# Performance work log

Measured on AMD Instinct MI355X. Metric: run time of the kernel, lower is better.

Reference implementation:

```python
import jax, jax.numpy as jnp
import numpy as np

B, T, S, D, H = 2, 2048, 2048, 2048, 16
HD = D // H  # 128
SCALE = 1.0 / np.sqrt(HD)


def _rope(x, cos, sin):
    # x: [B,H,S,HD]; cos/sin: [1,1,S,HD//2]
    b, h, s, d = x.shape
    xs = x.reshape(b, h, s, d // 2, 2)
    x0, x1 = xs[..., 0], xs[..., 1]
    rot = jnp.stack([x0 * cos - x1 * sin, x1 * cos + x0 * sin], axis=-1)
    return rot.reshape(b, h, s, d)


def _split_heads(x):
    b, s, _ = x.shape
    return x.reshape(b, s, H, HD).transpose(0, 2, 1, 3)


def setup_inputs() -> dict:
    key = jax.random.key(0)
    ks = jax.random.split(key, 6)
    w_std = (1.0 / np.sqrt(2.0)) * np.sqrt(6.0 / (D + D))  # xavier_uniform with gain 1/sqrt(2)
    def xavier(k):
        return jax.random.uniform(k, (D, D), jnp.float32, -w_std, w_std)
    # rotary tables (standard inv-freq form)
    inv_freq = 1.0 / (10000.0 ** (np.arange(0, HD, 2, dtype=np.float32) / HD))  # [HD//2]
    ang = np.arange(T, dtype=np.float32)[:, None] * inv_freq[None, :]           # [T,HD//2]
    cos = jnp.asarray(np.cos(ang), jnp.float32)[None, None]  # [1,1,T,HD//2]
    sin = jnp.asarray(np.sin(ang), jnp.float32)[None, None]
    return {
        "hidden_states": jax.random.normal(ks[0], (B, T, D), jnp.float32),
        "encoder_hidden_states": jax.random.normal(ks[1], (B, S, D), jnp.float32),
        "Wq": xavier(ks[2]),
        "Wk": xavier(ks[3]),
        "Wv": xavier(ks[4]),
        "Wo": xavier(ks[5]),
        "cos_q": cos, "sin_q": sin,
        "cos_k": cos, "sin_k": sin,
    }


def reference(hidden_states, encoder_hidden_states, Wq, Wk, Wv, Wo,
              cos_q, sin_q, cos_k, sin_k):
    # Linear (no bias): y = x @ W.T
    q = _split_heads(jnp.einsum('btd,ed->bte', hidden_states, Wq))          # [B,H,T,HD]
    k = _split_heads(jnp.einsum('bsd,ed->bse', encoder_hidden_states, Wk))  # [B,H,S,HD]
    v = _split_heads(jnp.einsum('bsd,ed->bse', encoder_hidden_states, Wv))  # [B,H,S,HD]
    q = _rope(q, cos_q, sin_q)
    k = _rope(k, cos_k, sin_k)
    scores = jnp.einsum('bhtd,bhsd->bhts', q, k) * SCALE                    # [B,H,T,S]
    attn = jax.nn.softmax(scores.astype(jnp.float32), axis=-1)
    ctx = jnp.einsum('bhts,bhsd->bhtd', attn, v)                            # [B,H,T,HD]
    ctx = ctx.transpose(0, 2, 1, 3).reshape(B, T, D)                        # merge heads
    return jnp.einsum('btd,ed->bte', ctx, Wo)
```

## Files before the change

### kernel.cpp

```cpp
#include <hip/hip_runtime.h>
#include <cmath>

#define SCALE_F 0.088388347648318447f

typedef _Float16 f16;
typedef _Float16 f16x8 __attribute__((ext_vector_type(8)));
typedef _Float16 f16x4 __attribute__((ext_vector_type(4)));
typedef float f32x4 __attribute__((ext_vector_type(4)));
typedef float f32x16 __attribute__((ext_vector_type(16)));
typedef unsigned int u32;
typedef unsigned int u32x4 __attribute__((ext_vector_type(4)));

#define MFMA16(a, b, c) __builtin_amdgcn_mfma_f32_16x16x32_f16(a, b, c, 0, 0, 0)
#define MFMA32(a, b, c) __builtin_amdgcn_mfma_f32_32x32x16_f16(a, b, c, 0, 0, 0)
#define Z16 ((f32x16){0.f,0.f,0.f,0.f,0.f,0.f,0.f,0.f,0.f,0.f,0.f,0.f,0.f,0.f,0.f,0.f})

__device__ __forceinline__ void gl2lds16(const f16* g, f16* l) {
    __builtin_amdgcn_global_load_lds(
        (const __attribute__((address_space(1))) unsigned int*)g,
        (__attribute__((address_space(3))) unsigned int*)l, 16, 0, 0);
}

__device__ __forceinline__ u32 pk2(float x, float y) {
    const unsigned short a = __builtin_bit_cast(unsigned short, (f16)x);
    const unsigned short b = __builtin_bit_cast(unsigned short, (f16)y);
    return (u32)a | ((u32)b << 16);
}
__device__ __forceinline__ float fswapsum(float x) {
    u32 a = __builtin_bit_cast(u32, x), b;
    asm volatile("v_mov_b32 %0, %1" : "=&v"(b) : "v"(a));
    asm volatile("v_permlane32_swap_b32 %0, %1" : "+v"(a), "+v"(b));
    return __builtin_bit_cast(float, a) + __builtin_bit_cast(float, b);
}
__device__ __forceinline__ float fswapmax(float x) {
    u32 a = __builtin_bit_cast(u32, x), b;
    asm volatile("v_mov_b32 %0, %1" : "=&v"(b) : "v"(a));
    asm volatile("v_permlane32_swap_b32 %0, %1" : "+v"(a), "+v"(b));
    return fmaxf(__builtin_bit_cast(float, a), __builtin_bit_cast(float, b));
}

__global__ __launch_bounds__(256) void cvt_all(
    const float* __restrict__ hs, const float* __restrict__ es,
    const float* __restrict__ Wq, const float* __restrict__ Wk,
    const float* __restrict__ Wv, const float* __restrict__ Wo,
    f16* __restrict__ dst)
{
    const int c = blockIdx.x * 256 + threadIdx.x;
    const float* src; int off;
    if (c < 2097152) { src = (c < 1048576) ? hs : es; off = c & 1048575; }
    else {
        const int cc = c - 2097152;
        const int wsel = cc >> 19; off = cc & 524287;
        src = wsel == 0 ? Wq : wsel == 1 ? Wk : wsel == 2 ? Wv : Wo;
    }
    const float4* p = (const float4*)src + (size_t)off * 2;
    const float4 a = p[0], b2 = p[1];
    f16x8 o = {(f16)a.x, (f16)a.y, (f16)a.z, (f16)a.w,
               (f16)b2.x, (f16)b2.y, (f16)b2.z, (f16)b2.w};
    *(f16x8*)(dst + (size_t)c * 8) = o;
}

template <int OUT_MODE>
__global__ __launch_bounds__(256, 2) void gemm16(
    const f16* __restrict__ A, const f16* __restrict__ W,
    void* __restrict__ Cv, int M, int N, int K,
    const float* __restrict__ Cs, const float* __restrict__ Sn)
{
    __shared__ __align__(16) f16 Al[128 * 64];
    __shared__ __align__(16) f16 Bl[128 * 64];
    const int tid = threadIdx.x;
    const int l = tid & 63, w = tid >> 6;
    const int wr = w >> 1, wc = w & 1;

    const int nwg = gridDim.x, cpx = nwg >> 3;
    const int bid = blockIdx.x;
    const int swz = (bid & 7) * cpx + (bid >> 3);
    const int nbn = N >> 7;
    const int bm = (swz / nbn) * 128, bn = (swz % nbn) * 128;

    f32x4 acc[4][4];
#pragma unroll
    for (int i = 0; i < 4; ++i)
#pragma unroll
        for (int j = 0; j < 4; ++j) acc[i][j] = (f32x4){0.f, 0.f, 0.f, 0.f};

    const int srow = tid >> 3;
    const int sg = tid & 7;

    for (int k0 = 0; k0 < K; k0 += 64) {
        __syncthreads();
#pragma unroll
        for (int i = 0; i < 4; ++i) {
            const int row = i * 32 + srow;
            const int lg = sg ^ (row & 7);
            gl2lds16(A + (size_t)(bm + row) * K + k0 + lg * 8, Al + row * 64 + sg * 8);
            gl2lds16(W + (size_t)(bn + row) * K + k0 + lg * 8, Bl + row * 64 + sg * 8);
        }
        __syncthreads();
#pragma unroll
        for (int kk = 0; kk < 2; ++kk) {
            f16x8 a[4], b[4];
            const int g = kk * 4 + (l >> 4);
#pragma unroll
            for (int m = 0; m < 4; ++m) {
                const int row = wr * 64 + m * 16 + (l & 15);
                a[m] = *(const f16x8*)(Al + row * 64 + (g ^ (row & 7)) * 8);
            }
#pragma unroll
            for (int n = 0; n < 4; ++n) {
                const int row = wc * 64 + n * 16 + (l & 15);
                b[n] = *(const f16x8*)(Bl + row * 64 + (g ^ (row & 7)) * 8);
            }
#pragma unroll
            for (int m = 0; m < 4; ++m)
#pragma unroll
                for (int n = 0; n < 4; ++n)
                    acc[m][n] = MFMA16(a[m], b[n], acc[m][n]);
        }
    }

#pragma unroll
    for (int m = 0; m < 4; ++m)
#pragma unroll
        for (int n = 0; n < 4; ++n)
#pragma unroll
            for (int j = 0; j < 4; ++j) {
                const int r = bm + wr * 64 + m * 16 + ((l >> 4) << 2) + j;
                const int c = bn + wc * 64 + n * 16 + (l & 15);
                if (OUT_MODE == 0) {
                    ((f16*)Cv)[(size_t)r * N + c] = (f16)acc[m][n][j];
                } else if (OUT_MODE == 2) {
                    ((float*)Cv)[(size_t)r * N + c] = acc[m][n][j];
                } else if (OUT_MODE == 3) {
                    ((f16*)Cv)[(size_t)((c >> 11) * 2048 + r) * 2048 + (c & 2047)] = (f16)acc[m][n][j];
                } else if (OUT_MODE == 4) {
                    const float v = acc[m][n][j];
                    const float vp = __shfl_xor(v, 1);
                    const int t = r & 2047;
                    const int i2 = (c & 127) >> 1;
                    const float co = Cs[t * 64 + i2];
                    const float si = Sn[t * 64 + i2];
                    const float y = (c & 1) ? fmaf(v, co, vp * si) : fmaf(v, co, -vp * si);
                    ((f16*)Cv)[(size_t)r * N + c] = (f16)y;
                }
            }
}

__global__ __launch_bounds__(512, 1) void attn16(
    const f16* __restrict__ Qg, const f16* __restrict__ Kg,
    const f16* __restrict__ Vt, f16* __restrict__ Og)
{
    __shared__ __align__(16) f16 Kl[2][64 * 128];
    __shared__ __align__(16) f16 Vl[2][128 * 64];
    __shared__ float bnc[8][32];

    const int tid = threadIdx.x;
    const int l = tid & 63, w = tid >> 6;
    const int l31 = l & 31, hi = l >> 5;
    const int hi4 = hi * 4;

    const int bid = blockIdx.x;
    const int swz = (bid & 7) * 32 + (bid >> 3);
    const int bh = swz >> 3, qt = swz & 7;
    const int b = bh >> 4, h = bh & 15;

    const int qrow = b * 2048 + qt * 256 + w * 32 + l31;
    const f16 qsc = (f16)(0.088388347648318447f * 1.44269504088896f);
    f16x8 qf[8];
#pragma unroll
    for (int kc = 0; kc < 8; ++kc) {
        f16x8 t0 = *(const f16x8*)(Qg + (size_t)qrow * 2048 + h * 128 + kc * 16 + hi * 8);
#pragma unroll
        for (int e = 0; e < 8; ++e) t0[e] = t0[e] * qsc;
        qf[kc] = t0;
    }

    f32x16 o[4] = {Z16, Z16, Z16, Z16};
    float mrow = -3.0e38f, lrow = 0.0f;

    const f16* Kbase = Kg + (size_t)(b * 2048) * 2048 + h * 128;
    const f16* Vbase = Vt + (size_t)(b * 2048 + h * 128) * 2048;

#define STAGE(buf, st) do {                                                              \
    _Pragma("unroll")                                                                    \
    for (int u = 0; u < 2; ++u) {                                                        \
        const int idx = u * 512 + tid; const int row = idx >> 4, g = idx & 15;           \
        gl2lds16(Kbase + (size_t)((st) + row) * 2048 + (g ^ (row & 15)) * 8,             \
                 &Kl[buf][row * 128 + g * 8]);                                           \
    }                                                                                    \
    _Pragma("unroll")                                                                    \
    for (int u = 0; u < 2; ++u) {                                                        \
        const int idx = u * 512 + tid; const int d = idx >> 3, g = idx & 7;              \
        gl2lds16(Vbase + (size_t)d * 2048 + (st) + (g ^ (d & 7)) * 8,                    \
                 &Vl[buf][d * 64 + g * 8]);                                              \
    }                                                                                    \
} while (0)

    STAGE(0, 0);
    __syncthreads();

    int cur = 0;
    for (int t = 0; t < 32; ++t) {
        if (t < 31) STAGE(cur ^ 1, (t + 1) * 64);
        const f16* Kc = Kl[cur];
        const f16* Vc = Vl[cur];

        f32x16 p0 = Z16, p1 = Z16;
        __builtin_amdgcn_s_setprio(1);
#pragma unroll
        for (int kc = 0; kc < 8; ++kc) {
            const int g = ((kc * 2 + hi) ^ (l31 & 15)) * 8;
            const f16x8 k0 = *(const f16x8*)(Kc + l31 * 128 + g);
            const f16x8 k1 = *(const f16x8*)(Kc + (32 + l31) * 128 + g);
            p0 = MFMA32(k0, qf[kc], p0);
            p1 = MFMA32(k1, qf[kc], p1);
        }
        __builtin_amdgcn_s_setprio(0);

        float mx = fmaxf(p0[0], p1[0]);
#pragma unroll
        for (int r = 1; r < 16; ++r) mx = fmaxf(mx, fmaxf(p0[r], p1[r]));
        mx = fswapmax(mx);

        if (!__all(mx <= mrow + 8.0f)) {
            const float mn = fmaxf(mrow, mx);
            const float cr = exp2f(mrow - mn);
            mrow = mn;
            lrow *= cr;
            if (hi == 0) bnc[w][l31] = cr;
#pragma unroll
            for (int r = 0; r < 16; ++r) {
                const float crr = bnc[w][(r & 3) + 8 * (r >> 2) + 4 * hi];
                o[0][r] *= crr; o[1][r] *= crr; o[2][r] *= crr; o[3][r] *= crr;
            }
        }

        float s0 = 0.f, s1 = 0.f, s2 = 0.f, s3 = 0.f;
#pragma unroll
        for (int r = 0; r < 16; r += 4) {
            p0[r]     = exp2f(p0[r]     - mrow); s0 += p0[r];
            p0[r + 1] = exp2f(p0[r + 1] - mrow); s1 += p0[r + 1];
            p0[r + 2] = exp2f(p0[r + 2] - mrow); s2 += p0[r + 2];
            p0[r + 3] = exp2f(p0[r + 3] - mrow); s3 += p0[r + 3];
        }
#pragma unroll
        for (int r = 0; r < 16; r += 4) {
            p1[r]     = exp2f(p1[r]     - mrow); s0 += p1[r];
            p1[r + 1] = exp2f(p1[r + 1] - mrow); s1 += p1[r + 1];
            p1[r + 2] = exp2f(p1[r + 2] - mrow); s2 += p1[r + 2];
            p1[r + 3] = exp2f(p1[r + 3] - mrow); s3 += p1[r + 3];
        }
        lrow += fswapsum((s0 + s1) + (s2 + s3));

        f16x8 pf[4];
#pragma unroll
        for (int ksl = 0; ksl < 2; ++ksl) {
            u32x4 w0 = {pk2(p0[8*ksl+0], p0[8*ksl+1]), pk2(p0[8*ksl+2], p0[8*ksl+3]),
                        pk2(p0[8*ksl+4], p0[8*ksl+5]), pk2(p0[8*ksl+6], p0[8*ksl+7])};
            pf[ksl] = __builtin_bit_cast(f16x8, w0);
            u32x4 w1 = {pk2(p1[8*ksl+0], p1[8*ksl+1]), pk2(p1[8*ksl+2], p1[8*ksl+3]),
                        pk2(p1[8*ksl+4], p1[8*ksl+5]), pk2(p1[8*ksl+6], p1[8*ksl+7])};
            pf[2 + ksl] = __builtin_bit_cast(f16x8, w1);
        }

        __builtin_amdgcn_s_setprio(1);
#pragma unroll
        for (int dt = 0; dt < 4; ++dt) {
            const f16* vrow = Vc + (dt * 32 + l31) * 64;
#pragma unroll
            for (int ks = 0; ks < 4; ++ks) {
                const f16x4 vlo = *(const f16x4*)(vrow + ((ks * 2)     ^ (l31 & 7)) * 8 + hi4);
                const f16x4 vhi = *(const f16x4*)(vrow + ((ks * 2 + 1) ^ (l31 & 7)) * 8 + hi4);
                const f16x8 vf = __builtin_shufflevector(vlo, vhi, 0, 1, 2, 3, 4, 5, 6, 7);
                o[dt] = MFMA32(pf[ks], vf, o[dt]);
            }
        }
        __builtin_amdgcn_s_setprio(0);

        __syncthreads();
        cur ^= 1;
    }
#undef STAGE

    const float inv = 1.0f / lrow;
    if (hi == 0) bnc[w][l31] = inv;
#pragma unroll
    for (int r = 0; r < 16; ++r) {
        const int qq = (r & 3) + 8 * (r >> 2) + 4 * hi;
        const float ir = bnc[w][qq];
        const size_t row = (size_t)(b * 2048 + qt * 256 + w * 32 + qq);
#pragma unroll
        for (int dt = 0; dt < 4; ++dt)
            Og[row * 2048 + h * 128 + dt * 32 + l31] = (f16)(o[dt][r] * ir);
    }
}

extern "C" void kernel_launch(void* const* d_in, const int* in_sizes, int n_in,
                              void* d_out, int out_size, void* d_ws, size_t ws_size,
                              hipStream_t stream) {
    const float* hs = (const float*)d_in[0];
    const float* es = (const float*)d_in[1];
    const float* Wq = (const float*)d_in[2];
    const float* Wk = (const float*)d_in[3];
    const float* Wv = (const float*)d_in[4];
    const float* Wo = (const float*)d_in[5];
    const float* cq = (const float*)d_in[6];
    const float* sq = (const float*)d_in[7];
    const float* ck = (const float*)d_in[8];
    const float* sk = (const float*)d_in[9];
    float* out = (float*)d_out;

    f16* hs16 = (f16*)d_ws;
    f16* es16 = hs16 + 8388608;
    f16* Wq16 = es16 + 8388608;
    f16* Wk16 = Wq16 + 4194304;
    f16* Wv16 = Wk16 + 4194304;
    f16* Wo16 = Wv16 + 4194304;
    f16* Q16  = Wo16 + 4194304;
    f16* K16  = Q16 + 8388608;
    f16* Vt16 = K16 + 8388608;
    f16* ctx16 = hs16;

    const dim3 tB(256);
    cvt_all<<<dim3(16384), tB, 0, stream>>>(hs, es, Wq, Wk, Wv, Wo, hs16);

    gemm16<4><<<dim3(512), tB, 0, stream>>>(hs16, Wq16, Q16, 4096, 2048, 2048, cq, sq);
    gemm16<4><<<dim3(512), tB, 0, stream>>>(es16, Wk16, K16, 4096, 2048, 2048, ck, sk);
    gemm16<3><<<dim3(512), tB, 0, stream>>>(Wv16, es16, Vt16, 2048, 4096, 2048, nullptr, nullptr);

    attn16<<<dim3(256), dim3(512), 0, stream>>>(Q16, K16, Vt16, ctx16);

    gemm16<2><<<dim3(512), tB, 0, stream>>>(ctx16, Wo16, out, 4096, 2048, 2048, nullptr, nullptr);
}
```

Measured before the change: 303.9 us.

## Shrink attention blocks to 4 waves, two per CU, and use native exp2

The attention kernel now launches 512 blocks of 256 threads, each covering 128 query rows instead of 256, with launch bounds allowing two resident blocks per CU. This is meant to give finer-grained scheduling and overlap between blocks, at the cost of loading each K/V tile once per 128 query rows instead of once per 256, which doubles K/V traffic. The row max and row sum reductions become tree-shaped to shorten dependency chains, and exp2f is replaced by the hardware exp2 builtin to skip library range handling.

```diff
diff --git a/kernel.cpp b/kernel.cpp
--- a/kernel.cpp
+++ b/kernel.cpp
@@ -14,6 +14,7 @@
 #define MFMA16(a, b, c) __builtin_amdgcn_mfma_f32_16x16x32_f16(a, b, c, 0, 0, 0)
 #define MFMA32(a, b, c) __builtin_amdgcn_mfma_f32_32x32x16_f16(a, b, c, 0, 0, 0)
 #define Z16 ((f32x16){0.f,0.f,0.f,0.f,0.f,0.f,0.f,0.f,0.f,0.f,0.f,0.f,0.f,0.f,0.f,0.f})
+#define EX2(x) __builtin_amdgcn_exp2f(x)
 
 __device__ __forceinline__ void gl2lds16(const f16* g, f16* l) {
     __builtin_amdgcn_global_load_lds(
@@ -146,13 +147,13 @@
             }
 }
 
-__global__ __launch_bounds__(512, 1) void attn16(
+__global__ __launch_bounds__(256, 2) void attn16(
     const f16* __restrict__ Qg, const f16* __restrict__ Kg,
     const f16* __restrict__ Vt, f16* __restrict__ Og)
 {
     __shared__ __align__(16) f16 Kl[2][64 * 128];
     __shared__ __align__(16) f16 Vl[2][128 * 64];
-    __shared__ float bnc[8][32];
+    __shared__ float bnc[4][32];
 
     const int tid = threadIdx.x;
     const int l = tid & 63, w = tid >> 6;
@@ -160,11 +161,11 @@
     const int hi4 = hi * 4;
 
     const int bid = blockIdx.x;
-    const int swz = (bid & 7) * 32 + (bid >> 3);
-    const int bh = swz >> 3, qt = swz & 7;
+    const int swz = (bid & 7) * 64 + (bid >> 3);
+    const int bh = swz >> 4, qt = swz & 15;
     const int b = bh >> 4, h = bh & 15;
 
-    const int qrow = b * 2048 + qt * 256 + w * 32 + l31;
+    const int qrow = b * 2048 + qt * 128 + w * 32 + l31;
     const f16 qsc = (f16)(0.088388347648318447f * 1.44269504088896f);
     f16x8 qf[8];
 #pragma unroll
@@ -183,14 +184,14 @@
 
 #define STAGE(buf, st) do {                                                              \
     _Pragma("unroll")                                                                    \
-    for (int u = 0; u < 2; ++u) {                                                        \
-        const int idx = u * 512 + tid; const int row = idx >> 4, g = idx & 15;           \
+    for (int u = 0; u < 4; ++u) {                                                        \
+        const int idx = u * 256 + tid; const int row = idx >> 4, g = idx & 15;           \
         gl2lds16(Kbase + (size_t)((st) + row) * 2048 + (g ^ (row & 15)) * 8,             \
                  &Kl[buf][row * 128 + g * 8]);                                           \
     }                                                                                    \
     _Pragma("unroll")                                                                    \
-    for (int u = 0; u < 2; ++u) {                                                        \
-        const int idx = u * 512 + tid; const int d = idx >> 3, g = idx & 7;              \
+    for (int u = 0; u < 4; ++u) {                                                        \
+        const int idx = u * 256 + tid; const int d = idx >> 3, g = idx & 7;              \
         gl2lds16(Vbase + (size_t)d * 2048 + (st) + (g ^ (d & 7)) * 8,                    \
                  &Vl[buf][d * 64 + g * 8]);                                              \
     }                                                                                    \
@@ -217,14 +218,19 @@
         }
         __builtin_amdgcn_s_setprio(0);
 
-        float mx = fmaxf(p0[0], p1[0]);
-#pragma unroll
-        for (int r = 1; r < 16; ++r) mx = fmaxf(mx, fmaxf(p0[r], p1[r]));
+        float mt[16];
+#pragma unroll
+        for (int r = 0; r < 16; ++r) mt[r] = fmaxf(p0[r], p1[r]);
+#pragma unroll
+        for (int r = 0; r < 8; ++r) mt[r] = fmaxf(mt[r], mt[r + 8]);
+#pragma unroll
+        for (int r = 0; r < 4; ++r) mt[r] = fmaxf(mt[r], mt[r + 4]);
+        float mx = fmaxf(fmaxf(mt[0], mt[1]), fmaxf(mt[2], mt[3]));
         mx = fswapmax(mx);
 
         if (!__all(mx <= mrow + 8.0f)) {
             const float mn = fmaxf(mrow, mx);
-            const float cr = exp2f(mrow - mn);
+            const float cr = EX2(mrow - mn);
             mrow = mn;
             lrow *= cr;
             if (hi == 0) bnc[w][l31] = cr;
@@ -235,22 +241,18 @@
             }
         }
 
-        float s0 = 0.f, s1 = 0.f, s2 = 0.f, s3 = 0.f;
-#pragma unroll
-        for (int r = 0; r < 16; r += 4) {
-            p0[r]     = exp2f(p0[r]     - mrow); s0 += p0[r];
-            p0[r + 1] = exp2f(p0[r + 1] - mrow); s1 += p0[r + 1];
-            p0[r + 2] = exp2f(p0[r + 2] - mrow); s2 += p0[r + 2];
-            p0[r + 3] = exp2f(p0[r + 3] - mrow); s3 += p0[r + 3];
-        }
-#pragma unroll
-        for (int r = 0; r < 16; r += 4) {
-            p1[r]     = exp2f(p1[r]     - mrow); s0 += p1[r];
-            p1[r + 1] = exp2f(p1[r + 1] - mrow); s1 += p1[r + 1];
-            p1[r + 2] = exp2f(p1[r + 2] - mrow); s2 += p1[r + 2];
-            p1[r + 3] = exp2f(p1[r + 3] - mrow); s3 += p1[r + 3];
-        }
-        lrow += fswapsum((s0 + s1) + (s2 + s3));
+        float st16[16];
+#pragma unroll
+        for (int r = 0; r < 16; ++r) {
+            p0[r] = EX2(p0[r] - mrow);
+            p1[r] = EX2(p1[r] - mrow);
+            st16[r] = p0[r] + p1[r];
+        }
+#pragma unroll
+        for (int r = 0; r < 8; ++r) st16[r] += st16[r + 8];
+#pragma unroll
+        for (int r = 0; r < 4; ++r) st16[r] += st16[r + 4];
+        lrow += fswapsum((st16[0] + st16[1]) + (st16[2] + st16[3]));
 
         f16x8 pf[4];
 #pragma unroll
@@ -288,7 +290,7 @@
     for (int r = 0; r < 16; ++r) {
         const int qq = (r & 3) + 8 * (r >> 2) + 4 * hi;
         const float ir = bnc[w][qq];
-        const size_t row = (size_t)(b * 2048 + qt * 256 + w * 32 + qq);
+        const size_t row = (size_t)(b * 2048 + qt * 128 + w * 32 + qq);
 #pragma unroll
         for (int dt = 0; dt < 4; ++dt)
             Og[row * 2048 + h * 128 + dt * 32 + l31] = (f16)(o[dt][r] * ir);
@@ -328,7 +330,7 @@
     gemm16<4><<<dim3(512), tB, 0, stream>>>(es16, Wk16, K16, 4096, 2048, 2048, ck, sk);
     gemm16<3><<<dim3(512), tB, 0, stream>>>(Wv16, es16, Vt16, 2048, 4096, 2048, nullptr, nullptr);
 
-    attn16<<<dim3(256), dim3(512), 0, stream>>>(Q16, K16, Vt16, ctx16);
+    attn16<<<dim3(512), tB, 0, stream>>>(Q16, K16, Vt16, ctx16);
 
     gemm16<2><<<dim3(512), tB, 0, stream>>>(ctx16, Wo16, out, 4096, 2048, 2048, nullptr, nullptr);
 }
```

Measured after the change: 292.6 us. 3.7% less time.
